# Performance work log

Hardware: AMD Instinct MI355X
Metric: run time of the kernel (lower is better)

Reference implementation:

```python
import jax, jax.numpy as jnp
import numpy as np

THRESHOLD = 1.0  # LIF firing threshold (single-step LIF: spike = heaviside(v - thr))


def _lif_spike(v):
    # single-step LIF: membrane = input, spike where membrane exceeds threshold
    return (v > THRESHOLD).astype(v.dtype)


def setup_inputs() -> dict:
    key = jax.random.key(0)
    ks = jax.random.split(key, 9)
    B, T, C = 2, 2048, 1024
    s = 1.0 / np.sqrt(C)
    return {
        "x": jax.random.normal(ks[0], (B, T, C), dtype=jnp.float32),
        "Wq": jax.random.normal(ks[1], (C, C), dtype=jnp.float32) * s,
        "bq": jnp.zeros((C,), dtype=jnp.float32),
        "Wk": jax.random.normal(ks[2], (C, C), dtype=jnp.float32) * s,
        "bk": jnp.zeros((C,), dtype=jnp.float32),
        "Wv": jax.random.normal(ks[3], (C, C), dtype=jnp.float32) * s,
        "bv": jnp.zeros((C,), dtype=jnp.float32),
        "Wo": jax.random.normal(ks[4], (C, C), dtype=jnp.float32) * s,
        "bo": jnp.zeros((C,), dtype=jnp.float32),
    }


def reference(x, Wq, bq, Wk, bk, Wv, bv, Wo, bo):
    B, T, C = x.shape
    H = 16
    D = C // H
    q = x @ Wq.T + bq
    k = x @ Wk.T + bk
    v = x @ Wv.T + bv
    # LIF spiking on q and k (binary spikes)
    qs = _lif_spike(q).reshape(B, T, H, D).transpose(0, 2, 1, 3)  # [B,H,T,D]
    ks = _lif_spike(k).reshape(B, T, H, D).transpose(0, 2, 1, 3)  # [B,H,T,D]
    vh = v.reshape(B, T, H, D).transpose(0, 2, 1, 3)              # [B,H,T,D]
    scores = jnp.einsum('bhqd,bhkd->bhqk', qs, ks) / jnp.sqrt(jnp.asarray(D, x.dtype))
    attn = jax.nn.softmax(scores, axis=-1)
    out = jnp.einsum('bhqk,bhkd->bhqd', attn, vh)                 # [B,H,T,D]
    out = out.transpose(0, 2, 1, 3).reshape(B, T, C)
    return out @ Wo.T + bo
```

## Files before the change

### kernel.cpp

```cpp
#include <hip/hip_runtime.h>
#include <cstdint>

typedef unsigned long long u64;
typedef unsigned int u32;
typedef unsigned short u16;
typedef __attribute__((ext_vector_type(8))) u16 u16x8;
typedef __attribute__((ext_vector_type(4))) u16 u16x4;
typedef __attribute__((ext_vector_type(8))) _Float16 f16x8;
typedef __attribute__((ext_vector_type(4))) float f32x4;

#define T_LEN 2048
#define C_DIM 1024
#define H_NUM 16
#define M_ROWS 4096
#define MB (1024ull * 1024ull)
#define TAU 3e-3f
#define FCAP 65536u
#define BLK_FCAP 512u

__device__ __forceinline__ u16 f2bf(float f) {
  unsigned u = __builtin_bit_cast(unsigned, f);
  return (u16)((u + 0x7FFFu + ((u >> 16) & 1u)) >> 16);
}
__device__ __forceinline__ u16 f2h(float f) {
  _Float16 h = (_Float16)f;
  return __builtin_bit_cast(u16, h);
}

__device__ __forceinline__ void async16(u16* lds, const u16* g) {
  __builtin_amdgcn_global_load_lds(
      (const __attribute__((address_space(1))) void*)g,
      (__attribute__((address_space(3))) void*)lds, 16, 0, 0);
}

__global__ __launch_bounds__(256) void split_all(
    const float* __restrict__ x,  const float* __restrict__ Wq,
    const float* __restrict__ Wk, const float* __restrict__ Wv,
    const float* __restrict__ Wo,
    u16* xh, u16* wq16, u16* wk16, u16* wv16, u16* woh, u32* flagcnt)
{
  const int i = blockIdx.x * 256 + threadIdx.x;
  if (i == 0) *flagcnt = 0;
  const float* src; u16* dst; int off; int isbf = 0;
  if      (i < 1048576) { src = x;  dst = xh;   off = i; }
  else if (i < 1310720) { src = Wq; dst = wq16; off = i - 1048576; }
  else if (i < 1572864) { src = Wk; dst = wk16; off = i - 1310720; }
  else if (i < 1835008) { src = Wv; dst = wv16; off = i - 1572864; }
  else                  { src = Wo; dst = woh;  off = i - 1835008; isbf = 1; }
  const float4 v = ((const float4*)src)[off];
  u16x4 h;
  if (isbf) {
    h[0] = f2bf(v.x); h[1] = f2bf(v.y); h[2] = f2bf(v.z); h[3] = f2bf(v.w);
  } else {
    h[0] = f2h(v.x);  h[1] = f2h(v.y);  h[2] = f2h(v.z);  h[3] = f2h(v.w);
  }
  ((u16x4*)dst)[off] = h;
}

__global__ __launch_bounds__(256) void mfma_qkv(
    const u16* __restrict__ A16,
    const u16* __restrict__ Bq16, const u16* __restrict__ Bk16,
    const u16* __restrict__ Bv16,
    const float* __restrict__ bq, const float* __restrict__ bk,
    const float* __restrict__ bv,
    u32* __restrict__ pbits, u32* __restrict__ flagcnt,
    u32* __restrict__ flaglist, u16* __restrict__ vT)
{
  __shared__ u16 Ahs[2][128][32];
  __shared__ u16 Bqs[2][64][32];
  __shared__ u16 Bks[2][64][32];
  __shared__ u16 Bvs[2][64][32];
  __shared__ u32 fls[2 + BLK_FCAP];

  const int tid  = threadIdx.x;
  const int lane = tid & 63;
  const int w    = tid >> 6;
  const int wr   = w & 1;
  const int wc   = w >> 1;
  const int bm   = blockIdx.x * 128;
  const int bn   = blockIdx.y * 64;

  if (tid == 0) fls[0] = 0;

  f32x4 acc[3][4][2];
  #pragma unroll
  for (int s = 0; s < 3; ++s)
    #pragma unroll
    for (int mf = 0; mf < 4; ++mf)
      #pragma unroll
      for (int nf = 0; nf < 2; ++nf) acc[s][mf][nf] = (f32x4){0.f, 0.f, 0.f, 0.f};

  const int sr = lane >> 2;
  const int sc = lane & 3;

#define STG(DST, SRC, TB, R0, KT)                                          \
  async16(&DST[(R0)][0],                                                   \
          &SRC[(size_t)((TB) + (R0) + sr) * 1024 + (KT) +                  \
               ((sc ^ ((((R0) + sr) >> 1) & 3)) << 3)]);

#define STAGE(B_, KT)                        \
  {                                          \
    STG(Ahs[B_], A16, bm, w * 32, KT);       \
    STG(Ahs[B_], A16, bm, w * 32 + 16, KT);  \
    STG(Bqs[B_], Bq16, bn, w * 16, KT);      \
    STG(Bks[B_], Bk16, bn, w * 16, KT);      \
    STG(Bvs[B_], Bv16, bn, w * 16, KT);      \
  }

  STAGE(0, 0);
  __syncthreads();

  const int fr = lane & 15;
  const int fg = lane >> 4;
  int cur = 0;

  for (int kt = 0; kt < 1024; kt += 32) {
    if (kt + 32 < 1024) STAGE(cur ^ 1, kt + 32);

    f16x8 a_h[4];
    #pragma unroll
    for (int mf = 0; mf < 4; ++mf) {
      const int row = wr * 64 + mf * 16 + fr;
      const int cs = (fg ^ ((row >> 1) & 3)) << 3;
      a_h[mf] = __builtin_bit_cast(f16x8, *(const u16x8*)&Ahs[cur][row][cs]);
    }
    const int col = wc * 32 + fr;
    const int cs0 = (fg ^ (((wc * 32 + fr) >> 1) & 3)) << 3;
    const int cs1 = (fg ^ (((wc * 32 + 16 + fr) >> 1) & 3)) << 3;
    (void)col;

    {
      f16x8 b0 = __builtin_bit_cast(f16x8, *(const u16x8*)&Bqs[cur][wc * 32 + fr][cs0]);
      f16x8 b1 = __builtin_bit_cast(f16x8, *(const u16x8*)&Bqs[cur][wc * 32 + 16 + fr][cs1]);
      #pragma unroll
      for (int mf = 0; mf < 4; ++mf) {
        acc[0][mf][0] = __builtin_amdgcn_mfma_f32_16x16x32_f16(a_h[mf], b0, acc[0][mf][0], 0, 0, 0);
        acc[0][mf][1] = __builtin_amdgcn_mfma_f32_16x16x32_f16(a_h[mf], b1, acc[0][mf][1], 0, 0, 0);
      }
    }
    {
      f16x8 b0 = __builtin_bit_cast(f16x8, *(const u16x8*)&Bks[cur][wc * 32 + fr][cs0]);
      f16x8 b1 = __builtin_bit_cast(f16x8, *(const u16x8*)&Bks[cur][wc * 32 + 16 + fr][cs1]);
      #pragma unroll
      for (int mf = 0; mf < 4; ++mf) {
        acc[1][mf][0] = __builtin_amdgcn_mfma_f32_16x16x32_f16(a_h[mf], b0, acc[1][mf][0], 0, 0, 0);
        acc[1][mf][1] = __builtin_amdgcn_mfma_f32_16x16x32_f16(a_h[mf], b1, acc[1][mf][1], 0, 0, 0);
      }
    }
    {
      f16x8 b0 = __builtin_bit_cast(f16x8, *(const u16x8*)&Bvs[cur][wc * 32 + fr][cs0]);
      f16x8 b1 = __builtin_bit_cast(f16x8, *(const u16x8*)&Bvs[cur][wc * 32 + 16 + fr][cs1]);
      #pragma unroll
      for (int mf = 0; mf < 4; ++mf) {
        acc[2][mf][0] = __builtin_amdgcn_mfma_f32_16x16x32_f16(a_h[mf], b0, acc[2][mf][0], 0, 0, 0);
        acc[2][mf][1] = __builtin_amdgcn_mfma_f32_16x16x32_f16(a_h[mf], b1, acc[2][mf][1], 0, 0, 0);
      }
    }
    __syncthreads();
    cur ^= 1;
  }
#undef STAGE
#undef STG

  const int head = bn >> 6;
  #pragma unroll
  for (int sel = 0; sel < 2; ++sel) {
    const float* bias = sel ? bk : bq;
    const int c0 = bn + wc * 32 + fr;
    const int c1 = c0 + 16;
    const float bb0 = bias[c0];
    const float bb1 = bias[c1];
    #pragma unroll
    for (int mf = 0; mf < 4; ++mf) {
      const int row0 = bm + wr * 64 + mf * 16;
      #pragma unroll
      for (int j = 0; j < 4; ++j) {
        const float v0 = acc[sel][mf][0][j] + bb0;
        const float v1 = acc[sel][mf][1][j] + bb1;
        const u64 b0 = __ballot(v0 > 1.0f);
        const u64 b1 = __ballot(v1 > 1.0f);
        const int m = row0 + fg * 4 + j;
        if (fr == 0) {
          const u32 mask = (u32)((b0 >> (fg * 16)) & 0xFFFFu)
                         | ((u32)((b1 >> (fg * 16)) & 0xFFFFu) << 16);
          pbits[(((size_t)sel * 4096 + m) * 16 + head) * 2 + wc] = mask;
        }
        if (__builtin_fabsf(v0 - 1.0f) < TAU) {
          const u32 s = atomicAdd(&fls[0], 1u);
          if (s < BLK_FCAP) fls[2 + s] = ((u32)sel << 22) | ((u32)m << 10) | (u32)c0;
        }
        if (__builtin_fabsf(v1 - 1.0f) < TAU) {
          const u32 s = atomicAdd(&fls[0], 1u);
          if (s < BLK_FCAP) fls[2 + s] = ((u32)sel << 22) | ((u32)m << 10) | (u32)c1;
        }
      }
    }
  }
  __syncthreads();
  {
    const u32 cnt = fls[0] < BLK_FCAP ? fls[0] : BLK_FCAP;
    if (tid == 0) fls[1] = atomicAdd(flagcnt, cnt);
    __syncthreads();
    const u32 base = fls[1];
    for (u32 i = tid; i < cnt; i += 256) {
      const u32 pos = base + i;
      if (pos < FCAP) flaglist[pos] = fls[2 + i];
    }
  }

  #pragma unroll
  for (int mf = 0; mf < 4; ++mf) {
    const int row0 = bm + wr * 64 + mf * 16 + fg * 4;
    #pragma unroll
    for (int nf = 0; nf < 2; ++nf) {
      const int col = bn + wc * 32 + nf * 16 + fr;
      const float bbv = bv[col];
      const int bb_ = row0 >> 11, t0 = row0 & 2047;
      const int hh = col >> 6, dd = col & 63;
      u16x4 o;
      o[0] = f2bf(acc[2][mf][nf][0] + bbv);
      o[1] = f2bf(acc[2][mf][nf][1] + bbv);
      o[2] = f2bf(acc[2][mf][nf][2] + bbv);
      o[3] = f2bf(acc[2][mf][nf][3] + bbv);
      *(u16x4*)&vT[(((size_t)(bb_ * 16 + hh)) * 64 + dd) * 2048 + t0] = o;
    }
  }
}

__global__ __launch_bounds__(256) void fix_bits(
    const float* __restrict__ x,
    const float* __restrict__ Wq, const float* __restrict__ Wk,
    const float* __restrict__ bq, const float* __restrict__ bk,
    u32* __restrict__ pbits,
    const u32* __restrict__ flagcnt, const u32* __restrict__ flaglist)
{
  u32 cnt = *flagcnt;
  if (cnt > FCAP) cnt = FCAP;
  const int lane = threadIdx.x & 63;
  const u32 wid  = (blockIdx.x * 256 + threadIdx.x) >> 6;
  const u32 nw   = gridDim.x * 4;
  for (u32 i = wid; i < cnt; i += nw) {
    const u32 e = flaglist[i];
    const int which = e >> 22;
    const int m = (e >> 10) & 4095;
    const int n = e & 1023;
    const float* W    = which ? Wk : Wq;
    const float* bias = which ? bk : bq;
    float s = 0.f;
    #pragma unroll
    for (int j = 0; j < 16; ++j)
      s += x[(size_t)m * 1024 + lane + j * 64] * W[(size_t)n * 1024 + lane + j * 64];
    #pragma unroll
    for (int off = 32; off > 0; off >>= 1) s += __shfl_xor(s, off);
    const float val = s + bias[n];
    if (lane == 0) {
      const size_t idx = (((size_t)which * 4096 + m) * 16 + (n >> 6)) * 2 + ((n >> 5) & 1);
      const u32 bit = 1u << (n & 31);
      const bool oldb = (pbits[idx] >> (n & 31)) & 1u;
      const bool newb = val > 1.0f;
      if (oldb != newb) atomicXor(&pbits[idx], bit);
    }
  }
}

__global__ __launch_bounds__(256) void attn_mfma(
    const u32* __restrict__ pbits, const u16* __restrict__ vT,
    u16* __restrict__ oh)
{
  __shared__ u16 vtb[64][72];
  __shared__ u64 kbt[68];
  __shared__ u32 wt_tab[65];

  const int tid = threadIdx.x, lane = tid & 63, w = tid >> 6;
  const int bid = ((blockIdx.x & 7) << 7) | (blockIdx.x >> 3);
  const int qt = bid & 31, bh = bid >> 5, b = bh >> 4, h = bh & 15;

  const int fr = lane & 15, fg = lane >> 4;

  if (tid < 65)
    wt_tab[tid] = __builtin_bit_cast(u32, exp2f((float)tid * 0.1803368801f));

  const int qm = b * T_LEN + qt * 64 + w * 16 + fr;
  const size_t qbase = (((size_t)qm) * 16 + h) * 2;
  const u32 qlo = pbits[qbase];
  const u32 qhi = pbits[qbase + 1];

  f32x4 acc[4];
  #pragma unroll
  for (int nf = 0; nf < 4; ++nf) acc[nf] = (f32x4){0.f, 0.f, 0.f, 0.f};
  f32x4 acc_z = (f32x4){0.f, 0.f, 0.f, 0.f};

  u16x8 ones;
  #pragma unroll
  for (int j = 0; j < 8; ++j) ones[j] = 0x3F80;

  const u16* vbase = vT + (size_t)bh * 64 * T_LEN;
  const int sd = tid >> 2, sk = (tid & 3) << 3;

  u16x8 r0, r1;
  u64 kbr = 0;
#define VLOAD(KT)                                                       \
  {                                                                     \
    r0 = *(const u16x8*)&vbase[(size_t)sd * T_LEN + (KT) + sk];         \
    r1 = *(const u16x8*)&vbase[(size_t)sd * T_LEN + (KT) + sk + 32];    \
  }
#define KLOAD(KT)                                                       \
  if (tid < 64) {                                                       \
    const int km = b * T_LEN + (KT) + tid;                              \
    const size_t kb = (((size_t)(4096 + km)) * 16 + h) * 2;             \
    kbr = (u64)pbits[kb] | ((u64)pbits[kb + 1] << 32);                  \
  }

  VLOAD(0);
  KLOAD(0);

  for (int kt = 0; kt < T_LEN; kt += 64) {
    *(u16x8*)&vtb[sd][sk]      = r0;
    *(u16x8*)&vtb[sd][sk + 32] = r1;
    if (tid < 64) kbt[tid + (tid >> 4)] = kbr;
    if (kt + 64 < T_LEN) { VLOAD(kt + 64); KLOAD(kt + 64); }
    __syncthreads();

    __builtin_amdgcn_s_setprio(1);
    #pragma unroll
    for (int ks = 0; ks < 2; ++ks) {
      u16x8 af;
      u32* afw = (u32*)&af;
      #pragma unroll
      for (int p = 0; p < 4; ++p) {
        const int kk = ks * 32 + fg * 8 + p * 2;
        const int pidx = kk + (kk >> 4);
        const u64 kb0 = kbt[pidx];
        const u64 kb1 = kbt[pidx + 1];
        const int mm0 = __builtin_popcount(qlo & (u32)kb0)
                      + __builtin_popcount(qhi & (u32)(kb0 >> 32));
        const int mm1 = __builtin_popcount(qlo & (u32)kb1)
                      + __builtin_popcount(qhi & (u32)(kb1 >> 32));
        const u32 t0 = wt_tab[mm0];
        const u32 t1 = wt_tab[mm1];
        afw[p] = (t1 & 0xFFFF0000u) | (t0 >> 16);
      }
      #pragma unroll
      for (int nf = 0; nf < 4; ++nf) {
        const u16x8 bfv = *(const u16x8*)&vtb[nf * 16 + fr][ks * 32 + fg * 8];
        acc[nf] = __builtin_amdgcn_mfma_f32_16x16x32_bf16(af, bfv, acc[nf], 0, 0, 0);
      }
      acc_z = __builtin_amdgcn_mfma_f32_16x16x32_bf16(af, ones, acc_z, 0, 0, 0);
    }
    __builtin_amdgcn_s_setprio(0);
    __syncthreads();
  }
#undef VLOAD
#undef KLOAD

  float invZ[4];
  #pragma unroll
  for (int j = 0; j < 4; ++j) invZ[j] = 1.0f / acc_z[j];

  #pragma unroll
  for (int nf = 0; nf < 4; ++nf) {
    const int col = h * 64 + nf * 16 + fr;
    #pragma unroll
    for (int j = 0; j < 4; ++j) {
      const int qrow = w * 16 + fg * 4 + j;
      const float o = acc[nf][j] * invZ[j];
      const size_t gq = (size_t)b * T_LEN + qt * 64 + qrow;
      oh[gq * 1024 + col] = f2bf(o);
    }
  }
}

__global__ __launch_bounds__(256) void mfma_out(
    const u16* __restrict__ Ah, const u16* __restrict__ Bh,
    const float* __restrict__ bias, float* __restrict__ out)
{
  __shared__ u16 Ahs[2][128][32];
  __shared__ u16 Bhs[2][64][32];

  const int tid  = threadIdx.x;
  const int lane = tid & 63;
  const int w    = tid >> 6;
  const int wr   = w & 1;
  const int wc   = w >> 1;
  const int bm   = blockIdx.x * 128;
  const int bn   = blockIdx.y * 64;

  f32x4 acc[4][2];
  #pragma unroll
  for (int mf = 0; mf < 4; ++mf)
    #pragma unroll
    for (int nf = 0; nf < 2; ++nf) acc[mf][nf] = (f32x4){0.f, 0.f, 0.f, 0.f};

  const int sr = lane >> 2;
  const int sc = lane & 3;

#define STG(DST, SRC, TB, R0, KT)                                          \
  async16(&DST[(R0)][0],                                                   \
          &SRC[(size_t)((TB) + (R0) + sr) * 1024 + (KT) +                  \
               ((sc ^ ((((R0) + sr) >> 1) & 3)) << 3)]);

#define STAGE(B_, KT)                        \
  {                                          \
    STG(Ahs[B_], Ah, bm, w * 32, KT);        \
    STG(Ahs[B_], Ah, bm, w * 32 + 16, KT);   \
    STG(Bhs[B_], Bh, bn, w * 16, KT);        \
  }

  STAGE(0, 0);
  __syncthreads();

  const int fr = lane & 15;
  const int fg = lane >> 4;
  int cur = 0;

  for (int kt = 0; kt < 1024; kt += 32) {
    if (kt + 32 < 1024) STAGE(cur ^ 1, kt + 32);

    u16x8 a_h[4], b_h[2];
    #pragma unroll
    for (int mf = 0; mf < 4; ++mf) {
      const int row = wr * 64 + mf * 16 + fr;
      const int cs = (fg ^ ((row >> 1) & 3)) << 3;
      a_h[mf] = *(const u16x8*)&Ahs[cur][row][cs];
    }
    #pragma unroll
    for (int nf = 0; nf < 2; ++nf) {
      const int col = wc * 32 + nf * 16 + fr;
      const int cs = (fg ^ ((col >> 1) & 3)) << 3;
      b_h[nf] = *(const u16x8*)&Bhs[cur][col][cs];
    }
    #pragma unroll
    for (int mf = 0; mf < 4; ++mf)
      #pragma unroll
      for (int nf = 0; nf < 2; ++nf)
        acc[mf][nf] = __builtin_amdgcn_mfma_f32_16x16x32_bf16(a_h[mf], b_h[nf], acc[mf][nf], 0, 0, 0);
    __syncthreads();
    cur ^= 1;
  }
#undef STAGE
#undef STG

  #pragma unroll
  for (int mf = 0; mf < 4; ++mf) {
    const int row0 = bm + wr * 64 + mf * 16 + fg * 4;
    #pragma unroll
    for (int nf = 0; nf < 2; ++nf) {
      const int col = bn + wc * 32 + nf * 16 + fr;
      const float bb = bias[col];
      #pragma unroll
      for (int j = 0; j < 4; ++j)
        out[(size_t)(row0 + j) * 1024 + col] = acc[mf][nf][j] + bb;
    }
  }
}

extern "C" void kernel_launch(void* const* d_in, const int* in_sizes, int n_in,
                              void* d_out, int out_size, void* d_ws, size_t ws_size,
                              hipStream_t stream) {
  const float* x  = (const float*)d_in[0];
  const float* Wq = (const float*)d_in[1];
  const float* bq = (const float*)d_in[2];
  const float* Wk = (const float*)d_in[3];
  const float* bk = (const float*)d_in[4];
  const float* Wv = (const float*)d_in[5];
  const float* bv = (const float*)d_in[6];
  const float* Wo = (const float*)d_in[7];
  const float* bo = (const float*)d_in[8];
  float* out = (float*)d_out;

  char* ws = (char*)d_ws;
  u16* oh   = (u16*)ws;
  u16* xh   = (u16*)(ws + 16 * MB);
  u16* vT   = (u16*)(ws + 32 * MB);
  u16* Woh  = (u16*)(ws + 40 * MB);
  u32* pbits = (u32*)(ws + 44 * MB);
  u32* flagcnt  = (u32*)(ws + 45 * MB);
  u32* flaglist = (u32*)(ws + 45 * MB + 256);

  char* dob = (char*)d_out;
  u16* Wq16 = (u16*)dob;
  u16* Wk16 = (u16*)(dob + 2 * MB);
  u16* Wv16 = (u16*)(dob + 4 * MB);

  split_all<<<8192, 256, 0, stream>>>(x, Wq, Wk, Wv, Wo,
                                      xh, Wq16, Wk16, Wv16, Woh, flagcnt);

  dim3 g1(M_ROWS / 128, 1024 / 64);
  mfma_qkv<<<g1, 256, 0, stream>>>(xh, Wq16, Wk16, Wv16,
                                   bq, bk, bv, pbits, flagcnt, flaglist, vT);

  fix_bits<<<256, 256, 0, stream>>>(x, Wq, Wk, bq, bk, pbits, flagcnt, flaglist);

  attn_mfma<<<32 * 32, 256, 0, stream>>>(pbits, vT, oh);

  dim3 g2(M_ROWS / 128, 1024 / 64);
  mfma_out<<<g2, 256, 0, stream>>>(oh, Woh, bo, out);
}
```

Baseline: 145.4 us.

## Split attention key range in two and combine partials in separate kernel

The attention kernel now splits the 2048-key loop into two halves, launching 2048 blocks instead of 1024. Each block writes unnormalized bf16 partial outputs and fp32 row sums. A new combine kernel adds the two partials, divides by the total sum and writes the bf16 attention output. This doubles the grid to fill more compute units on the MI355X, at the cost of an extra launch, extra global traffic for the partials, and an extra bf16 rounding step.

```diff
diff --git a/kernel.cpp b/kernel.cpp
--- a/kernel.cpp
+++ b/kernel.cpp
@@ -21,6 +21,9 @@
 __device__ __forceinline__ u16 f2bf(float f) {
   unsigned u = __builtin_bit_cast(unsigned, f);
   return (u16)((u + 0x7FFFu + ((u >> 16) & 1u)) >> 16);
+}
+__device__ __forceinline__ float bf2f(u16 u) {
+  return __builtin_bit_cast(float, ((unsigned)u) << 16);
 }
 __device__ __forceinline__ u16 f2h(float f) {
   _Float16 h = (_Float16)f;
@@ -124,10 +127,8 @@
       const int cs = (fg ^ ((row >> 1) & 3)) << 3;
       a_h[mf] = __builtin_bit_cast(f16x8, *(const u16x8*)&Ahs[cur][row][cs]);
     }
-    const int col = wc * 32 + fr;
     const int cs0 = (fg ^ (((wc * 32 + fr) >> 1) & 3)) << 3;
     const int cs1 = (fg ^ (((wc * 32 + 16 + fr) >> 1) & 3)) << 3;
-    (void)col;
 
     {
       f16x8 b0 = __builtin_bit_cast(f16x8, *(const u16x8*)&Bqs[cur][wc * 32 + fr][cs0]);
@@ -265,15 +266,17 @@
 
 __global__ __launch_bounds__(256) void attn_mfma(
     const u32* __restrict__ pbits, const u16* __restrict__ vT,
-    u16* __restrict__ oh)
+    u16* __restrict__ po0, u16* __restrict__ po1, float* __restrict__ pz)
 {
   __shared__ u16 vtb[64][72];
   __shared__ u64 kbt[68];
   __shared__ u32 wt_tab[65];
 
   const int tid = threadIdx.x, lane = tid & 63, w = tid >> 6;
-  const int bid = ((blockIdx.x & 7) << 7) | (blockIdx.x >> 3);
-  const int qt = bid & 31, bh = bid >> 5, b = bh >> 4, h = bh & 15;
+  const int bid = ((blockIdx.x & 7) << 8) | (blockIdx.x >> 3);
+  const int qt = bid & 31, bh = (bid >> 5) & 31, s = bid >> 10;
+  const int b = bh >> 4, h = bh & 15;
+  const int kt0 = s << 10;
 
   const int fr = lane & 15, fg = lane >> 4;
 
@@ -311,14 +314,14 @@
     kbr = (u64)pbits[kb] | ((u64)pbits[kb + 1] << 32);                  \
   }
 
-  VLOAD(0);
-  KLOAD(0);
-
-  for (int kt = 0; kt < T_LEN; kt += 64) {
+  VLOAD(kt0);
+  KLOAD(kt0);
+
+  for (int kt = kt0; kt < kt0 + 1024; kt += 64) {
     *(u16x8*)&vtb[sd][sk]      = r0;
     *(u16x8*)&vtb[sd][sk + 32] = r1;
     if (tid < 64) kbt[tid + (tid >> 4)] = kbr;
-    if (kt + 64 < T_LEN) { VLOAD(kt + 64); KLOAD(kt + 64); }
+    if (kt + 64 < kt0 + 1024) { VLOAD(kt + 64); KLOAD(kt + 64); }
     __syncthreads();
 
     __builtin_amdgcn_s_setprio(1);
@@ -353,21 +356,46 @@
 #undef VLOAD
 #undef KLOAD
 
-  float invZ[4];
-  #pragma unroll
-  for (int j = 0; j < 4; ++j) invZ[j] = 1.0f / acc_z[j];
-
+  u16* po = s ? po1 : po0;
+  const int bidlin = (bh << 5) | qt;
   #pragma unroll
   for (int nf = 0; nf < 4; ++nf) {
-    const int col = h * 64 + nf * 16 + fr;
     #pragma unroll
     for (int j = 0; j < 4; ++j) {
       const int qrow = w * 16 + fg * 4 + j;
-      const float o = acc[nf][j] * invZ[j];
-      const size_t gq = (size_t)b * T_LEN + qt * 64 + qrow;
-      oh[gq * 1024 + col] = f2bf(o);
-    }
-  }
+      po[((size_t)bidlin * 64 + qrow) * 64 + nf * 16 + fr] = f2bf(acc[nf][j]);
+    }
+  }
+  if (fr == 0) {
+    #pragma unroll
+    for (int j = 0; j < 4; ++j) {
+      const int qrow = w * 16 + fg * 4 + j;
+      pz[(size_t)(s << 16) + bidlin * 64 + qrow] = acc_z[j];
+    }
+  }
+}
+
+__global__ __launch_bounds__(256) void combine(
+    const u16* __restrict__ po0, const u16* __restrict__ po1,
+    const float* __restrict__ pz, u16* __restrict__ oh)
+{
+  const int e = blockIdx.x * 256 + threadIdx.x;
+  const int d0 = (e & 15) << 2;
+  const int qrow = (e >> 4) & 63;
+  const int bidlin = e >> 10;
+  const float z = pz[bidlin * 64 + qrow] + pz[65536 + bidlin * 64 + qrow];
+  const float rz = 1.0f / z;
+  const size_t pbase = ((size_t)bidlin * 64 + qrow) * 64 + d0;
+  const u16x4 a  = *(const u16x4*)&po0[pbase];
+  const u16x4 b4 = *(const u16x4*)&po1[pbase];
+  u16x4 o;
+  #pragma unroll
+  for (int i = 0; i < 4; ++i)
+    o[i] = f2bf((bf2f(a[i]) + bf2f(b4[i])) * rz);
+  const int bh = bidlin >> 5, qt = bidlin & 31;
+  const int b = bh >> 4, h = bh & 15;
+  const size_t gq = (size_t)b * T_LEN + qt * 64 + qrow;
+  *(u16x4*)&oh[gq * 1024 + h * 64 + d0] = o;
 }
 
 __global__ __launch_bounds__(256) void mfma_out(
@@ -470,9 +498,12 @@
 
   char* ws = (char*)d_ws;
   u16* oh   = (u16*)ws;
+  u16* po1  = (u16*)(ws + 8 * MB);
   u16* xh   = (u16*)(ws + 16 * MB);
+  u16* po0  = (u16*)(ws + 24 * MB);
   u16* vT   = (u16*)(ws + 32 * MB);
   u16* Woh  = (u16*)(ws + 40 * MB);
+  float* pz = (float*)(ws + 42 * MB);
   u32* pbits = (u32*)(ws + 44 * MB);
   u32* flagcnt  = (u32*)(ws + 45 * MB);
   u32* flaglist = (u32*)(ws + 45 * MB + 256);
@@ -491,7 +522,9 @@
 
   fix_bits<<<256, 256, 0, stream>>>(x, Wq, Wk, bq, bk, pbits, flagcnt, flaglist);
 
-  attn_mfma<<<32 * 32, 256, 0, stream>>>(pbits, vT, oh);
+  attn_mfma<<<2048, 256, 0, stream>>>(pbits, vT, po0, po1, pz);
+
+  combine<<<4096, 256, 0, stream>>>(po0, po1, pz, oh);
 
   dim3 g2(M_ROWS / 128, 1024 / 64);
   mfma_out<<<g2, 256, 0, stream>>>(oh, Woh, bo, out);
```

New measurement: 152.9 us. +5.2%, slower.
